# Performance work log

Hardware: AMD Instinct MI355X
Metric: run time of the kernel (lower is better)

## Reference

```python
import jax, jax.numpy as jnp
import numpy as np

K = 10  # value-iteration steps


def _conv(x, w):
    # NCHW x OIHW -> NCHW, stride 1, SAME padding (pad=2 for 5x5, pad=0 for 1x1)
    return jax.lax.conv_general_dilated(
        x, w, window_strides=(1, 1), padding='SAME',
        dimension_numbers=('NCHW', 'OIHW', 'NCHW'))


def setup_inputs() -> dict:
    key = jax.random.key(0)
    ks = jax.random.split(key, 6)
    B, H, W = 64, 64, 64
    dim_h, n_hat, n_act = 150, 8, 4
    maze = jax.random.randint(ks[0], (B, H, W), 0, 3)
    # fixed embedding table from the torch module
    emb = jnp.array([[0.0, 0.0], [1.0, 0.0], [0.0, 10.0]], dtype=jnp.float32)
    encode_w = jax.random.normal(ks[1], (dim_h, 2, 5, 5), dtype=jnp.float32) * 0.05
    encode_b = jnp.zeros((dim_h,), dtype=jnp.float32)
    r_w = jax.random.normal(ks[2], (1, dim_h, 1, 1), dtype=jnp.float32) * 0.05
    q_w = jax.random.normal(ks[3], (n_hat, 1, 5, 5), dtype=jnp.float32) * 0.05
    # torch inits self.w to zeros; use small randn so the recurrence is non-trivial
    w = jax.random.normal(ks[4], (n_hat, 1, 5, 5), dtype=jnp.float32) * 0.05
    fc_w = jax.random.normal(ks[5], (n_act, n_hat), dtype=jnp.float32) * 0.1
    return dict(maze=maze, emb=emb, encode_w=encode_w, encode_b=encode_b,
                r_w=r_w, q_w=q_w, w=w, fc_w=fc_w)


def reference(maze, emb, encode_w, encode_b, r_w, q_w, w, fc_w):
    # embed: [B,H,W] -> [B,H,W,2] -> [B,2,H,W]
    m = emb[maze].transpose(0, 3, 1, 2)
    h = _conv(m, encode_w) + encode_b[None, :, None, None]  # [B,150,H,W]
    r = _conv(h, r_w)                                        # [B,1,H,W]
    q = _conv(r, q_w)                                        # [B,8,H,W]
    wk = jnp.concatenate([q_w, w], axis=1)                   # [8,2,5,5]

    def step(q, _):
        v = jnp.max(q, axis=1, keepdims=True)                # [B,1,H,W]
        q = _conv(jnp.concatenate([r, v], axis=1), wk)       # [B,8,H,W]
        return q, None

    q, _ = jax.lax.scan(step, q, None, length=K)
    q = q.transpose(0, 2, 3, 1)                              # [B,H,W,8]
    return q @ fc_w.T                                        # [B,H,W,4]
```

## Files before the change

kernel.cpp:

```cpp
#include <hip/hip_runtime.h>
#include <hip/hip_bf16.h>


#define NHAT 8
#define DIMH 150

typedef float v2f __attribute__((ext_vector_type(2)));

__global__ __launch_bounds__(128) void prep_kernel(
    const float* __restrict__ emb, const float* __restrict__ encode_w,
    const float* __restrict__ encode_b, const float* __restrict__ r_w,
    float* __restrict__ T, float* __restrict__ beff) {
  __shared__ float weff[2][25];
  int tid = threadIdx.x;
  if (tid < 50) {
    int i = tid / 25, k = tid % 25;
    float s = 0.f;
    for (int c = 0; c < DIMH; ++c)
      s += r_w[c] * encode_w[c * 50 + i * 25 + k];
    weff[i][k] = s;
  }
  if (tid == 64) {
    float s = 0.f;
    for (int c = 0; c < DIMH; ++c) s += r_w[c] * encode_b[c];
    *beff = s;
  }
  __syncthreads();
  if (tid < 100) {
    int val = tid / 25, k = tid % 25;
    float t = 0.f;
    if (val < 3) t = weff[0][k] * emb[val * 2] + weff[1][k] * emb[val * 2 + 1];
    T[val * 25 + k] = t;
  }
}

__global__ __launch_bounds__(512) void rq_kernel(
    const int* __restrict__ maze, const float* __restrict__ Tg,
    const float* __restrict__ beffg, const float* __restrict__ q_w,
    float* __restrict__ q0g) {
  __shared__ float Ts[4][25];
  __shared__ float bsh;
  __shared__ v2f qw2[25][4];
  __shared__ unsigned char mzt[24][68];
  __shared__ float rt[20][68];

  int tid = threadIdx.x;
  int b = blockIdx.y, A0 = blockIdx.x * 16;

  if (tid < 100) Ts[tid / 25][tid % 25] = Tg[tid];
  if (tid == 100) bsh = *beffg;
  if (tid >= 128 && tid < 228) {
    int t2 = tid - 128;
    int k = t2 >> 2, j = t2 & 3;
    qw2[k][j] = (v2f){q_w[(2 * j) * 25 + k], q_w[(2 * j + 1) * 25 + k]};
  }
  for (int i = tid; i < 24 * 68; i += 512) {
    int mr = i / 68, mc = i % 68;
    int gy = A0 - 4 + mr, gx = mc - 2;
    unsigned char v = 3;
    if (gy >= 0 && gy < 64 && gx >= 0 && gx < 64)
      v = (unsigned char)maze[(b * 64 + gy) * 64 + gx];
    mzt[mr][mc] = v;
  }
  __syncthreads();
  for (int i = tid; i < 20 * 68; i += 512) {
    int rr = i / 68, cc = i % 68;
    int gy = A0 - 2 + rr, gx = cc - 2;
    float v = 0.f;
    if (gy >= 0 && gy < 64 && gx >= 0 && gx < 64) {
      v = bsh;
#pragma unroll
      for (int ky = 0; ky < 5; ++ky)
#pragma unroll
        for (int kx = 0; kx < 5; ++kx)
          v += Ts[mzt[rr + ky][cc - 2 + kx]][ky * 5 + kx];
    }
    rt[rr][cc] = v;
  }
  __syncthreads();
  for (int i = tid; i < 16 * 64; i += 512) {
    int ly = i >> 6, gx = i & 63;
    int gy = A0 + ly;
    v2f acc[4];
#pragma unroll
    for (int j = 0; j < 4; ++j) acc[j] = (v2f){0.f, 0.f};
#pragma unroll
    for (int ky = 0; ky < 5; ++ky)
#pragma unroll
      for (int kx = 0; kx < 5; ++kx) {
        int k = ky * 5 + kx;
        float vv = rt[ly + ky][gx + kx];
        v2f vv2 = (v2f){vv, vv};
#pragma unroll
        for (int j = 0; j < 4; ++j) acc[j] += qw2[k][j] * vv2;
      }
    float* dst = q0g + ((size_t)(b * 4096 + gy * 64 + gx)) * NHAT;
    ((float4*)dst)[0] = make_float4(acc[0].x, acc[0].y, acc[1].x, acc[1].y);
    ((float4*)dst)[1] = make_float4(acc[2].x, acc[2].y, acc[3].x, acc[3].y);
  }
}

__global__ __launch_bounds__(512, 2) void vi_kernel(
    const float* __restrict__ q0g, const float* __restrict__ w,
    const float* __restrict__ fc_w, float* __restrict__ out) {
  __shared__ __align__(16) float vbuf[2][60][68];
  __shared__ __align__(16) float tmp[52][2][64];
  __shared__ v2f wl2[25][4];

  int tid = threadIdx.x;
  int b = blockIdx.y, a0 = blockIdx.x * 16;
  int wave = tid >> 6, lane = tid & 63;
  int half = wave & 1, slot = wave >> 1;
  int roff = lane >> 4, i4 = (lane & 15) * 4;

  if (tid < 100) {
    int k = tid >> 2, j = tid & 3;
    wl2[k][j] = (v2f){w[(2 * j) * 25 + k], w[(2 * j + 1) * 25 + k]};
  }
  for (int i = tid; i < 2 * 60 * 68; i += 512) ((float*)vbuf)[i] = 0.f;
  __syncthreads();

  v2f wr0[25], wr1[25];
#pragma unroll
  for (int k = 0; k < 25; ++k) {
    wr0[k] = wl2[k][2 * half];
    wr1[k] = wl2[k][2 * half + 1];
  }

  const float* q0b = q0g + (size_t)b * 4096 * NHAT;
  int cur = 0;

  {
    int s = max(0, a0 - 20), e = min(64, a0 + 36);
    int gx = lane;
    for (int r = s + wave; r < e; r += 8) {
      const float4* p = (const float4*)(q0b + ((size_t)r * 64 + gx) * NHAT);
      float4 f0 = p[0], f1 = p[1];
      float m = fmaxf(fmaxf(fmaxf(f0.x, f0.y), fmaxf(f0.z, f0.w)),
                      fmaxf(fmaxf(f1.x, f1.y), fmaxf(f1.z, f1.w)));
      vbuf[0][r - a0 + 22][gx + 2] = m;
    }
  }
  __syncthreads();

  for (int t = 1; t <= 9; ++t) {
    int hh = 2 * (10 - t);
    int s = max(0, a0 - hh), e = min(64, a0 + 16 + hh);
    for (int rb = s + 4 * slot; rb < e; rb += 16) {
      int r = rb + roff;
      if (r < e) {
        int lr = r - a0 + 22;
        const float4* qp =
            (const float4*)(q0b + ((size_t)r * 64 + i4) * NHAT + half * 4);
        float4 qv0 = qp[0], qv1 = qp[2], qv2 = qp[4], qv3 = qp[6];
        v2f aA[4], aB[4];
        aA[0] = (v2f){qv0.x, qv0.y}; aB[0] = (v2f){qv0.z, qv0.w};
        aA[1] = (v2f){qv1.x, qv1.y}; aB[1] = (v2f){qv1.z, qv1.w};
        aA[2] = (v2f){qv2.x, qv2.y}; aB[2] = (v2f){qv2.z, qv2.w};
        aA[3] = (v2f){qv3.x, qv3.y}; aB[3] = (v2f){qv3.z, qv3.w};
#pragma unroll
        for (int jj = 0; jj < 5; ++jj) {
          const float* row = &vbuf[cur][lr - 2 + jj][i4];
          float4 fa = *(const float4*)row;
          float4 fb = *(const float4*)(row + 4);
          float f[8] = {fa.x, fa.y, fa.z, fa.w, fb.x, fb.y, fb.z, fb.w};
#pragma unroll
          for (int kx = 0; kx < 5; ++kx) {
            int k = jj * 5 + kx;
            v2f w0 = wr0[k], w1 = wr1[k];
#pragma unroll
            for (int j = 0; j < 4; ++j) {
              v2f vv2 = (v2f){f[j + kx], f[j + kx]};
              aA[j] += w0 * vv2;
              aB[j] += w1 * vv2;
            }
          }
        }
        float m0 = fmaxf(fmaxf(aA[0].x, aA[0].y), fmaxf(aB[0].x, aB[0].y));
        float m1 = fmaxf(fmaxf(aA[1].x, aA[1].y), fmaxf(aB[1].x, aB[1].y));
        float m2 = fmaxf(fmaxf(aA[2].x, aA[2].y), fmaxf(aB[2].x, aB[2].y));
        float m3 = fmaxf(fmaxf(aA[3].x, aA[3].y), fmaxf(aB[3].x, aB[3].y));
        *(float4*)&tmp[lr - 4][half][i4] = make_float4(m0, m1, m2, m3);
      }
    }
    __syncthreads();
    int n = e - s;
    for (int idx = tid; idx < n * 64; idx += 512) {
      int rr = idx >> 6, px = idx & 63;
      int lr2 = s - a0 + 22 + rr;
      vbuf[cur ^ 1][lr2][px + 2] =
          fmaxf(tmp[lr2 - 4][0][px], tmp[lr2 - 4][1][px]);
    }
    __syncthreads();
    cur ^= 1;
  }

  float fcp[4][4];
#pragma unroll
  for (int a = 0; a < 4; ++a)
#pragma unroll
    for (int cc = 0; cc < 4; ++cc) fcp[a][cc] = fc_w[a * 8 + 4 * half + cc];
  float* ptmp = (float*)tmp;

  {
    int r = a0 + 4 * slot + roff;
    int lr = r - a0 + 22;
    const float4* qp =
        (const float4*)(q0b + ((size_t)r * 64 + i4) * NHAT + half * 4);
    float4 qv0 = qp[0], qv1 = qp[2], qv2 = qp[4], qv3 = qp[6];
    v2f aA[4], aB[4];
    aA[0] = (v2f){qv0.x, qv0.y}; aB[0] = (v2f){qv0.z, qv0.w};
    aA[1] = (v2f){qv1.x, qv1.y}; aB[1] = (v2f){qv1.z, qv1.w};
    aA[2] = (v2f){qv2.x, qv2.y}; aB[2] = (v2f){qv2.z, qv2.w};
    aA[3] = (v2f){qv3.x, qv3.y}; aB[3] = (v2f){qv3.z, qv3.w};
#pragma unroll
    for (int jj = 0; jj < 5; ++jj) {
      const float* row = &vbuf[cur][lr - 2 + jj][i4];
      float4 fa = *(const float4*)row;
      float4 fb = *(const float4*)(row + 4);
      float f[8] = {fa.x, fa.y, fa.z, fa.w, fb.x, fb.y, fb.z, fb.w};
#pragma unroll
      for (int kx = 0; kx < 5; ++kx) {
        int k = jj * 5 + kx;
        v2f w0 = wr0[k], w1 = wr1[k];
#pragma unroll
        for (int j = 0; j < 4; ++j) {
          v2f vv2 = (v2f){f[j + kx], f[j + kx]};
          aA[j] += w0 * vv2;
          aB[j] += w1 * vv2;
        }
      }
    }
    float4 pp[4];
#pragma unroll
    for (int j = 0; j < 4; ++j) {
      float q0v = aA[j].x, q1v = aA[j].y, q2v = aB[j].x, q3v = aB[j].y;
      pp[j].x = fcp[0][0] * q0v + fcp[0][1] * q1v + fcp[0][2] * q2v + fcp[0][3] * q3v;
      pp[j].y = fcp[1][0] * q0v + fcp[1][1] * q1v + fcp[1][2] * q2v + fcp[1][3] * q3v;
      pp[j].z = fcp[2][0] * q0v + fcp[2][1] * q1v + fcp[2][2] * q2v + fcp[2][3] * q3v;
      pp[j].w = fcp[3][0] * q0v + fcp[3][1] * q1v + fcp[3][2] * q2v + fcp[3][3] * q3v;
    }
    if (half == 1) {
#pragma unroll
      for (int j = 0; j < 4; ++j)
        *(float4*)&ptmp[(((r - a0) * 64) + i4 + j) * 4] = pp[j];
    }
    __syncthreads();
    if (half == 0) {
#pragma unroll
      for (int j = 0; j < 4; ++j) {
        float4 o = *(const float4*)&ptmp[(((r - a0) * 64) + i4 + j) * 4];
        o.x += pp[j].x; o.y += pp[j].y; o.z += pp[j].z; o.w += pp[j].w;
        *(float4*)&out[((size_t)((b * 64 + r) * 64 + i4 + j)) * 4] = o;
      }
    }
  }
}

extern "C" void kernel_launch(void* const* d_in, const int* in_sizes, int n_in,
                              void* d_out, int out_size, void* d_ws, size_t ws_size,
                              hipStream_t stream) {
  const int* maze = (const int*)d_in[0];
  const float* emb = (const float*)d_in[1];
  const float* encode_w = (const float*)d_in[2];
  const float* encode_b = (const float*)d_in[3];
  const float* r_w = (const float*)d_in[4];
  const float* q_w = (const float*)d_in[5];
  const float* w = (const float*)d_in[6];
  const float* fc_w = (const float*)d_in[7];
  float* out = (float*)d_out;

  float* wsf = (float*)d_ws;
  float* T = wsf;
  float* beff = wsf + 100;
  float* q0 = wsf + 128;

  prep_kernel<<<1, 128, 0, stream>>>(emb, encode_w, encode_b, r_w, T, beff);
  rq_kernel<<<dim3(4, 64), 512, 0, stream>>>(maze, T, beff, q_w, q0);
  vi_kernel<<<dim3(4, 64), 512, 0, stream>>>(q0, w, fc_w, out);
}
```

Before: 122.8 us.

## Fuse prep, reward/q0 and value-iteration kernels into one per-block kernel

Merges the three launches into a single kernel. Each block recomputes the effective encoder weights with a split reduction, builds the reward map for its 56-row halo window, and computes q0 into a private workspace slab laid out as [row][half][col][4] for the VI loop to read. This removes two kernel launches and the grid-wide dependency between q0 production and the VI stage. In exchange, each block redundantly recomputes the weight reduction and the overlapping halo rows of r and q0.

```diff
diff --git a/kernel.cpp b/kernel.cpp
--- a/kernel.cpp
+++ b/kernel.cpp
@@ -7,65 +7,91 @@
 
 typedef float v2f __attribute__((ext_vector_type(2)));
 
-__global__ __launch_bounds__(128) void prep_kernel(
-    const float* __restrict__ emb, const float* __restrict__ encode_w,
-    const float* __restrict__ encode_b, const float* __restrict__ r_w,
-    float* __restrict__ T, float* __restrict__ beff) {
+__global__ __launch_bounds__(512, 2) void nav_kernel(
+    const int* __restrict__ maze, const float* __restrict__ emb,
+    const float* __restrict__ encode_w, const float* __restrict__ encode_b,
+    const float* __restrict__ r_w, const float* __restrict__ q_w,
+    const float* __restrict__ w, const float* __restrict__ fc_w,
+    float* __restrict__ q0p_all, float* __restrict__ out) {
+  __shared__ __align__(16) float vbuf[2][60][68];
+  __shared__ __align__(16) float tmp[52][2][64];
+  __shared__ v2f wl2[25][4];
+  __shared__ float Ts[4][25];
+  __shared__ float bsh;
+  __shared__ float wpart[5][50];
+  __shared__ float bpart[152];
   __shared__ float weff[2][25];
+
   int tid = threadIdx.x;
+  int b = blockIdx.y, a0 = blockIdx.x * 16;
+  int bid = blockIdx.y * 4 + blockIdx.x;
+  int wave = tid >> 6, lane = tid & 63;
+  int half = wave & 1, slot = wave >> 1;
+  int roff = lane >> 4, i4 = (lane & 15) * 4;
+
+  float* q0p = q0p_all + (size_t)bid * (56 * 2 * 64 * 4);
+  unsigned char* mzt = (unsigned char*)&vbuf[0][0][0];
+  float* rt = &tmp[0][0][0];
+
+  if (tid < 100) {
+    int k = tid >> 2, j = tid & 3;
+    wl2[k][j] = (v2f){q_w[(2 * j) * 25 + k], q_w[(2 * j + 1) * 25 + k]};
+  }
+  if (tid >= 256 && tid < 506) {
+    int t2 = tid - 256;
+    int chunk = t2 / 50, ik = t2 % 50;
+    int i = ik / 25, k = ik % 25;
+    int c0 = chunk * 30;
+    float s = 0.f;
+    for (int c = c0; c < c0 + 30; ++c)
+      s += r_w[c] * encode_w[c * 50 + i * 25 + k];
+    wpart[chunk][ik] = s;
+  }
+  if (tid >= 100 && tid < 250) {
+    int c = tid - 100;
+    bpart[c] = r_w[c] * encode_b[c];
+  }
+  for (int i = tid; i < 64 * 68; i += 512) {
+    int mr = i / 68, mc = i % 68;
+    int gy = a0 - 24 + mr, gx = mc - 2;
+    unsigned char v = 3;
+    if (gy >= 0 && gy < 64 && gx >= 0 && gx < 64)
+      v = (unsigned char)maze[(b * 64 + gy) * 64 + gx];
+    mzt[mr * 68 + mc] = v;
+  }
+  __syncthreads();
+
+  v2f wr0[25], wr1[25];
+#pragma unroll
+  for (int k = 0; k < 25; ++k) {
+    wr0[k] = wl2[k][2 * half];
+    wr1[k] = wl2[k][2 * half + 1];
+  }
+
   if (tid < 50) {
-    int i = tid / 25, k = tid % 25;
     float s = 0.f;
-    for (int c = 0; c < DIMH; ++c)
-      s += r_w[c] * encode_w[c * 50 + i * 25 + k];
-    weff[i][k] = s;
-  }
-  if (tid == 64) {
+#pragma unroll
+    for (int ch = 0; ch < 5; ++ch) s += wpart[ch][tid];
+    weff[tid / 25][tid % 25] = s;
+  }
+  if (tid == 50) {
     float s = 0.f;
-    for (int c = 0; c < DIMH; ++c) s += r_w[c] * encode_b[c];
-    *beff = s;
-  }
-  __syncthreads();
+    for (int c = 0; c < 150; ++c) s += bpart[c];
+    bsh = s;
+  }
+  __syncthreads();
+
   if (tid < 100) {
     int val = tid / 25, k = tid % 25;
     float t = 0.f;
     if (val < 3) t = weff[0][k] * emb[val * 2] + weff[1][k] * emb[val * 2 + 1];
-    T[val * 25 + k] = t;
-  }
-}
-
-__global__ __launch_bounds__(512) void rq_kernel(
-    const int* __restrict__ maze, const float* __restrict__ Tg,
-    const float* __restrict__ beffg, const float* __restrict__ q_w,
-    float* __restrict__ q0g) {
-  __shared__ float Ts[4][25];
-  __shared__ float bsh;
-  __shared__ v2f qw2[25][4];
-  __shared__ unsigned char mzt[24][68];
-  __shared__ float rt[20][68];
-
-  int tid = threadIdx.x;
-  int b = blockIdx.y, A0 = blockIdx.x * 16;
-
-  if (tid < 100) Ts[tid / 25][tid % 25] = Tg[tid];
-  if (tid == 100) bsh = *beffg;
-  if (tid >= 128 && tid < 228) {
-    int t2 = tid - 128;
-    int k = t2 >> 2, j = t2 & 3;
-    qw2[k][j] = (v2f){q_w[(2 * j) * 25 + k], q_w[(2 * j + 1) * 25 + k]};
-  }
-  for (int i = tid; i < 24 * 68; i += 512) {
-    int mr = i / 68, mc = i % 68;
-    int gy = A0 - 4 + mr, gx = mc - 2;
-    unsigned char v = 3;
-    if (gy >= 0 && gy < 64 && gx >= 0 && gx < 64)
-      v = (unsigned char)maze[(b * 64 + gy) * 64 + gx];
-    mzt[mr][mc] = v;
-  }
-  __syncthreads();
-  for (int i = tid; i < 20 * 68; i += 512) {
+    Ts[val][k] = t;
+  }
+  __syncthreads();
+
+  for (int i = tid; i < 60 * 68; i += 512) {
     int rr = i / 68, cc = i % 68;
-    int gy = A0 - 2 + rr, gx = cc - 2;
+    int gy = a0 - 22 + rr, gx = cc - 2;
     float v = 0.f;
     if (gy >= 0 && gy < 64 && gx >= 0 && gx < 64) {
       v = bsh;
@@ -73,69 +99,71 @@
       for (int ky = 0; ky < 5; ++ky)
 #pragma unroll
         for (int kx = 0; kx < 5; ++kx)
-          v += Ts[mzt[rr + ky][cc - 2 + kx]][ky * 5 + kx];
-    }
-    rt[rr][cc] = v;
-  }
-  __syncthreads();
-  for (int i = tid; i < 16 * 64; i += 512) {
-    int ly = i >> 6, gx = i & 63;
-    int gy = A0 + ly;
-    v2f acc[4];
-#pragma unroll
-    for (int j = 0; j < 4; ++j) acc[j] = (v2f){0.f, 0.f};
-#pragma unroll
-    for (int ky = 0; ky < 5; ++ky)
-#pragma unroll
-      for (int kx = 0; kx < 5; ++kx) {
-        int k = ky * 5 + kx;
-        float vv = rt[ly + ky][gx + kx];
-        v2f vv2 = (v2f){vv, vv};
-#pragma unroll
-        for (int j = 0; j < 4; ++j) acc[j] += qw2[k][j] * vv2;
-      }
-    float* dst = q0g + ((size_t)(b * 4096 + gy * 64 + gx)) * NHAT;
-    ((float4*)dst)[0] = make_float4(acc[0].x, acc[0].y, acc[1].x, acc[1].y);
-    ((float4*)dst)[1] = make_float4(acc[2].x, acc[2].y, acc[3].x, acc[3].y);
-  }
-}
-
-__global__ __launch_bounds__(512, 2) void vi_kernel(
-    const float* __restrict__ q0g, const float* __restrict__ w,
-    const float* __restrict__ fc_w, float* __restrict__ out) {
-  __shared__ __align__(16) float vbuf[2][60][68];
-  __shared__ __align__(16) float tmp[52][2][64];
-  __shared__ v2f wl2[25][4];
-
-  int tid = threadIdx.x;
-  int b = blockIdx.y, a0 = blockIdx.x * 16;
-  int wave = tid >> 6, lane = tid & 63;
-  int half = wave & 1, slot = wave >> 1;
-  int roff = lane >> 4, i4 = (lane & 15) * 4;
+          v += Ts[mzt[(rr + ky) * 68 + (cc - 2 + kx)]][ky * 5 + kx];
+    }
+    rt[rr * 68 + cc] = v;
+  }
+  __syncthreads();
+
+  for (int rqb = 4 * slot; rqb < 56; rqb += 16) {
+    int rq = rqb + roff;
+    int gy = a0 - 20 + rq;
+    if (gy >= 0 && gy < 64) {
+      v2f aA[4], aB[4];
+#pragma unroll
+      for (int j = 0; j < 4; ++j) {
+        aA[j] = (v2f){0.f, 0.f};
+        aB[j] = (v2f){0.f, 0.f};
+      }
+#pragma unroll
+      for (int jj = 0; jj < 5; ++jj) {
+        const float* row = &rt[(rq + jj) * 68 + i4];
+        float4 fa = *(const float4*)row;
+        float4 fb = *(const float4*)(row + 4);
+        float f[8] = {fa.x, fa.y, fa.z, fa.w, fb.x, fb.y, fb.z, fb.w};
+#pragma unroll
+        for (int kx = 0; kx < 5; ++kx) {
+          int k = jj * 5 + kx;
+          v2f w0 = wr0[k], w1 = wr1[k];
+#pragma unroll
+          for (int j = 0; j < 4; ++j) {
+            v2f vv2 = (v2f){f[j + kx], f[j + kx]};
+            aA[j] += w0 * vv2;
+            aB[j] += w1 * vv2;
+          }
+        }
+      }
+#pragma unroll
+      for (int j = 0; j < 4; ++j) {
+        *(float4*)&q0p[(((size_t)rq * 2 + half) * 64 + i4 + j) * 4] =
+            make_float4(aA[j].x, aA[j].y, aB[j].x, aB[j].y);
+      }
+    }
+  }
+  __syncthreads();
 
   if (tid < 100) {
     int k = tid >> 2, j = tid & 3;
     wl2[k][j] = (v2f){w[(2 * j) * 25 + k], w[(2 * j + 1) * 25 + k]};
   }
-  for (int i = tid; i < 2 * 60 * 68; i += 512) ((float*)vbuf)[i] = 0.f;
-  __syncthreads();
-
-  v2f wr0[25], wr1[25];
+  __syncthreads();
 #pragma unroll
   for (int k = 0; k < 25; ++k) {
     wr0[k] = wl2[k][2 * half];
     wr1[k] = wl2[k][2 * half + 1];
   }
 
-  const float* q0b = q0g + (size_t)b * 4096 * NHAT;
+  for (int i = tid; i < 2 * 60 * 68; i += 512) ((float*)vbuf)[i] = 0.f;
+  __syncthreads();
+
   int cur = 0;
-
   {
     int s = max(0, a0 - 20), e = min(64, a0 + 36);
     int gx = lane;
     for (int r = s + wave; r < e; r += 8) {
-      const float4* p = (const float4*)(q0b + ((size_t)r * 64 + gx) * NHAT);
-      float4 f0 = p[0], f1 = p[1];
+      size_t rq = (size_t)(r - a0 + 20);
+      float4 f0 = *(const float4*)&q0p[((rq * 2 + 0) * 64 + gx) * 4];
+      float4 f1 = *(const float4*)&q0p[((rq * 2 + 1) * 64 + gx) * 4];
       float m = fmaxf(fmaxf(fmaxf(f0.x, f0.y), fmaxf(f0.z, f0.w)),
                       fmaxf(fmaxf(f1.x, f1.y), fmaxf(f1.z, f1.w)));
       vbuf[0][r - a0 + 22][gx + 2] = m;
@@ -151,8 +179,8 @@
       if (r < e) {
         int lr = r - a0 + 22;
         const float4* qp =
-            (const float4*)(q0b + ((size_t)r * 64 + i4) * NHAT + half * 4);
-        float4 qv0 = qp[0], qv1 = qp[2], qv2 = qp[4], qv3 = qp[6];
+            (const float4*)&q0p[(((size_t)(r - a0 + 20) * 2 + half) * 64 + i4) * 4];
+        float4 qv0 = qp[0], qv1 = qp[1], qv2 = qp[2], qv3 = qp[3];
         v2f aA[4], aB[4];
         aA[0] = (v2f){qv0.x, qv0.y}; aB[0] = (v2f){qv0.z, qv0.w};
         aA[1] = (v2f){qv1.x, qv1.y}; aB[1] = (v2f){qv1.z, qv1.w};
@@ -206,8 +234,8 @@
     int r = a0 + 4 * slot + roff;
     int lr = r - a0 + 22;
     const float4* qp =
-        (const float4*)(q0b + ((size_t)r * 64 + i4) * NHAT + half * 4);
-    float4 qv0 = qp[0], qv1 = qp[2], qv2 = qp[4], qv3 = qp[6];
+        (const float4*)&q0p[(((size_t)(r - a0 + 20) * 2 + half) * 64 + i4) * 4];
+    float4 qv0 = qp[0], qv1 = qp[1], qv2 = qp[2], qv3 = qp[3];
     v2f aA[4], aB[4];
     aA[0] = (v2f){qv0.x, qv0.y}; aB[0] = (v2f){qv0.z, qv0.w};
     aA[1] = (v2f){qv1.x, qv1.y}; aB[1] = (v2f){qv1.z, qv1.w};
@@ -270,12 +298,8 @@
   const float* fc_w = (const float*)d_in[7];
   float* out = (float*)d_out;
 
-  float* wsf = (float*)d_ws;
-  float* T = wsf;
-  float* beff = wsf + 100;
-  float* q0 = wsf + 128;
-
-  prep_kernel<<<1, 128, 0, stream>>>(emb, encode_w, encode_b, r_w, T, beff);
-  rq_kernel<<<dim3(4, 64), 512, 0, stream>>>(maze, T, beff, q_w, q0);
-  vi_kernel<<<dim3(4, 64), 512, 0, stream>>>(q0, w, fc_w, out);
+  float* q0p_all = (float*)d_ws;
+
+  nav_kernel<<<dim3(4, 64), 512, 0, stream>>>(
+      maze, emb, encode_w, encode_b, r_w, q_w, w, fc_w, q0p_all, out);
 }
```

New measurement: 125.8 us. 1.02x slower.

## Fuse weight-folding prep into rq kernel and split q0 into channel-half planes

Applied to the files above, without the earlier changes.

Removes the single-block prep kernel launch by having every rq block fold r_w into encode_w/encode_b itself, spread over many threads as partial sums followed by a reduction. The q0 workspace layout changes from 8 interleaved channels per pixel to two 4-channel half-planes per row, so each vi half-wave reads contiguous float4s instead of strided ones. This trades a serial launch and dependency for redundant weight-folding in each of 256 blocks and two extra barriers.

```diff
diff --git a/kernel.cpp b/kernel.cpp
--- a/kernel.cpp
+++ b/kernel.cpp
@@ -7,37 +7,14 @@
 
 typedef float v2f __attribute__((ext_vector_type(2)));
 
-__global__ __launch_bounds__(128) void prep_kernel(
-    const float* __restrict__ emb, const float* __restrict__ encode_w,
-    const float* __restrict__ encode_b, const float* __restrict__ r_w,
-    float* __restrict__ T, float* __restrict__ beff) {
+__global__ __launch_bounds__(512) void rq_kernel(
+    const int* __restrict__ maze, const float* __restrict__ emb,
+    const float* __restrict__ encode_w, const float* __restrict__ encode_b,
+    const float* __restrict__ r_w, const float* __restrict__ q_w,
+    float* __restrict__ q0g) {
+  __shared__ float wpart[5][50];
+  __shared__ float bpart[152];
   __shared__ float weff[2][25];
-  int tid = threadIdx.x;
-  if (tid < 50) {
-    int i = tid / 25, k = tid % 25;
-    float s = 0.f;
-    for (int c = 0; c < DIMH; ++c)
-      s += r_w[c] * encode_w[c * 50 + i * 25 + k];
-    weff[i][k] = s;
-  }
-  if (tid == 64) {
-    float s = 0.f;
-    for (int c = 0; c < DIMH; ++c) s += r_w[c] * encode_b[c];
-    *beff = s;
-  }
-  __syncthreads();
-  if (tid < 100) {
-    int val = tid / 25, k = tid % 25;
-    float t = 0.f;
-    if (val < 3) t = weff[0][k] * emb[val * 2] + weff[1][k] * emb[val * 2 + 1];
-    T[val * 25 + k] = t;
-  }
-}
-
-__global__ __launch_bounds__(512) void rq_kernel(
-    const int* __restrict__ maze, const float* __restrict__ Tg,
-    const float* __restrict__ beffg, const float* __restrict__ q_w,
-    float* __restrict__ q0g) {
   __shared__ float Ts[4][25];
   __shared__ float bsh;
   __shared__ v2f qw2[25][4];
@@ -47,12 +24,23 @@
   int tid = threadIdx.x;
   int b = blockIdx.y, A0 = blockIdx.x * 16;
 
-  if (tid < 100) Ts[tid / 25][tid % 25] = Tg[tid];
-  if (tid == 100) bsh = *beffg;
-  if (tid >= 128 && tid < 228) {
-    int t2 = tid - 128;
-    int k = t2 >> 2, j = t2 & 3;
+  if (tid < 100) {
+    int k = tid >> 2, j = tid & 3;
     qw2[k][j] = (v2f){q_w[(2 * j) * 25 + k], q_w[(2 * j + 1) * 25 + k]};
+  }
+  if (tid >= 256 && tid < 506) {
+    int t2 = tid - 256;
+    int chunk = t2 / 50, ik = t2 % 50;
+    int i = ik / 25, k = ik % 25;
+    int c0 = chunk * 30;
+    float s = 0.f;
+    for (int c = c0; c < c0 + 30; ++c)
+      s += r_w[c] * encode_w[c * 50 + i * 25 + k];
+    wpart[chunk][ik] = s;
+  }
+  if (tid >= 100 && tid < 250) {
+    int c = tid - 100;
+    bpart[c] = r_w[c] * encode_b[c];
   }
   for (int i = tid; i < 24 * 68; i += 512) {
     int mr = i / 68, mc = i % 68;
@@ -63,6 +51,25 @@
     mzt[mr][mc] = v;
   }
   __syncthreads();
+  if (tid < 50) {
+    float s = 0.f;
+#pragma unroll
+    for (int ch = 0; ch < 5; ++ch) s += wpart[ch][tid];
+    weff[tid / 25][tid % 25] = s;
+  }
+  if (tid == 50) {
+    float s = 0.f;
+    for (int c = 0; c < 150; ++c) s += bpart[c];
+    bsh = s;
+  }
+  __syncthreads();
+  if (tid < 100) {
+    int val = tid / 25, k = tid % 25;
+    float t = 0.f;
+    if (val < 3) t = weff[0][k] * emb[val * 2] + weff[1][k] * emb[val * 2 + 1];
+    Ts[val][k] = t;
+  }
+  __syncthreads();
   for (int i = tid; i < 20 * 68; i += 512) {
     int rr = i / 68, cc = i % 68;
     int gy = A0 - 2 + rr, gx = cc - 2;
@@ -94,9 +101,10 @@
 #pragma unroll
         for (int j = 0; j < 4; ++j) acc[j] += qw2[k][j] * vv2;
       }
-    float* dst = q0g + ((size_t)(b * 4096 + gy * 64 + gx)) * NHAT;
-    ((float4*)dst)[0] = make_float4(acc[0].x, acc[0].y, acc[1].x, acc[1].y);
-    ((float4*)dst)[1] = make_float4(acc[2].x, acc[2].y, acc[3].x, acc[3].y);
+    size_t base = ((size_t)(b * 64 + gy) * 2) * 64 + gx;
+    *(float4*)&q0g[(base)*4] = make_float4(acc[0].x, acc[0].y, acc[1].x, acc[1].y);
+    *(float4*)&q0g[(base + 64) * 4] =
+        make_float4(acc[2].x, acc[2].y, acc[3].x, acc[3].y);
   }
 }
 
@@ -127,15 +135,15 @@
     wr1[k] = wl2[k][2 * half + 1];
   }
 
-  const float* q0b = q0g + (size_t)b * 4096 * NHAT;
+  const float* q0b = q0g + (size_t)b * 64 * 2 * 64 * 4;
   int cur = 0;
 
   {
     int s = max(0, a0 - 20), e = min(64, a0 + 36);
     int gx = lane;
     for (int r = s + wave; r < e; r += 8) {
-      const float4* p = (const float4*)(q0b + ((size_t)r * 64 + gx) * NHAT);
-      float4 f0 = p[0], f1 = p[1];
+      float4 f0 = *(const float4*)&q0b[(((size_t)r * 2 + 0) * 64 + gx) * 4];
+      float4 f1 = *(const float4*)&q0b[(((size_t)r * 2 + 1) * 64 + gx) * 4];
       float m = fmaxf(fmaxf(fmaxf(f0.x, f0.y), fmaxf(f0.z, f0.w)),
                       fmaxf(fmaxf(f1.x, f1.y), fmaxf(f1.z, f1.w)));
       vbuf[0][r - a0 + 22][gx + 2] = m;
@@ -151,8 +159,8 @@
       if (r < e) {
         int lr = r - a0 + 22;
         const float4* qp =
-            (const float4*)(q0b + ((size_t)r * 64 + i4) * NHAT + half * 4);
-        float4 qv0 = qp[0], qv1 = qp[2], qv2 = qp[4], qv3 = qp[6];
+            (const float4*)&q0b[(((size_t)r * 2 + half) * 64 + i4) * 4];
+        float4 qv0 = qp[0], qv1 = qp[1], qv2 = qp[2], qv3 = qp[3];
         v2f aA[4], aB[4];
         aA[0] = (v2f){qv0.x, qv0.y}; aB[0] = (v2f){qv0.z, qv0.w};
         aA[1] = (v2f){qv1.x, qv1.y}; aB[1] = (v2f){qv1.z, qv1.w};
@@ -206,8 +214,8 @@
     int r = a0 + 4 * slot + roff;
     int lr = r - a0 + 22;
     const float4* qp =
-        (const float4*)(q0b + ((size_t)r * 64 + i4) * NHAT + half * 4);
-    float4 qv0 = qp[0], qv1 = qp[2], qv2 = qp[4], qv3 = qp[6];
+        (const float4*)&q0b[(((size_t)r * 2 + half) * 64 + i4) * 4];
+    float4 qv0 = qp[0], qv1 = qp[1], qv2 = qp[2], qv3 = qp[3];
     v2f aA[4], aB[4];
     aA[0] = (v2f){qv0.x, qv0.y}; aB[0] = (v2f){qv0.z, qv0.w};
     aA[1] = (v2f){qv1.x, qv1.y}; aB[1] = (v2f){qv1.z, qv1.w};
@@ -270,12 +278,9 @@
   const float* fc_w = (const float*)d_in[7];
   float* out = (float*)d_out;
 
-  float* wsf = (float*)d_ws;
-  float* T = wsf;
-  float* beff = wsf + 100;
-  float* q0 = wsf + 128;
-
-  prep_kernel<<<1, 128, 0, stream>>>(emb, encode_w, encode_b, r_w, T, beff);
-  rq_kernel<<<dim3(4, 64), 512, 0, stream>>>(maze, T, beff, q_w, q0);
-  vi_kernel<<<dim3(4, 64), 512, 0, stream>>>(q0, w, fc_w, out);
+  float* q0g = (float*)d_ws;
+
+  rq_kernel<<<dim3(4, 64), 512, 0, stream>>>(maze, emb, encode_w, encode_b,
+                                             r_w, q_w, q0g);
+  vi_kernel<<<dim3(4, 64), 512, 0, stream>>>(q0g, w, fc_w, out);
 }
```

Measured after the change: 114.5 us (median of 2 runs). 6.8% less time.
